# Kernel optimization log

Hardware: AMD Instinct MI355X
Metric: run time of the kernel (lower is better)

The kernel has to match this reference:

```python
import jax, jax.numpy as jnp
import numpy as np

DIM, NH, HD = 512, 16, 32   # dim, num_heads, head_dim = dim // num_heads
WH, WW = 8, 8               # window_size
SCALE = HD ** -0.5


def _rope2(t):
    """Axial 2D rotary embedding. t: (M, WH, WW, HD). First HD/2 dims rotate
    with the height position, last HD/2 with the width position."""
    d = HD // 2
    inv_freq = 1.0 / (10000.0 ** (jnp.arange(0, d, 2, dtype=jnp.float32) / d))  # (d/2,)

    def cos_sin(n):
        ang = jnp.arange(n, dtype=jnp.float32)[:, None] * inv_freq              # (n, d/2)
        return (jnp.concatenate([jnp.cos(ang)] * 2, -1),
                jnp.concatenate([jnp.sin(ang)] * 2, -1))                        # (n, d)

    def rot_half(u):
        u1, u2 = jnp.split(u, 2, axis=-1)
        return jnp.concatenate([-u2, u1], -1)

    cos_h, sin_h = cos_sin(WH)
    cos_w, sin_w = cos_sin(WW)
    th, tw = t[..., :d], t[..., d:]
    th = th * cos_h[:, None, :] + rot_half(th) * sin_h[:, None, :]
    tw = tw * cos_w[None, :, :] + rot_half(tw) * sin_w[None, :, :]
    return jnp.concatenate([th, tw], -1)


def setup_inputs() -> dict:
    key = jax.random.key(0)
    ks = jax.random.split(key, 8)
    s = 0.02
    return {
        "x": jax.random.normal(ks[0], (8, 64, 64, DIM), dtype=jnp.float32),
        "qkv_w": jax.random.normal(ks[1], (DIM, 3 * DIM), dtype=jnp.float32) * s,
        "qkv_b": jnp.zeros((3 * DIM,), dtype=jnp.float32),
        "kv_w": jax.random.normal(ks[2], (DIM, 2 * DIM), dtype=jnp.float32) * s,
        "kv_b": jnp.zeros((2 * DIM,), dtype=jnp.float32),
        "proj_w": jax.random.normal(ks[3], (DIM, DIM), dtype=jnp.float32) * s,
        "proj_b": jnp.zeros((DIM,), dtype=jnp.float32),
    }


def reference(x, qkv_w, qkv_b, kv_w, kv_b, proj_w, proj_b):
    B, H, W, C = x.shape
    # --- hydra linear-attention branch (computed in the torch module even when
    # use_attn=True, but its result is discarded on that path) ---
    hy_k, hy_v = jnp.split(x @ kv_w + kv_b, 2, axis=-1)
    hy_k = hy_k / jnp.linalg.norm(hy_k, axis=-1, keepdims=True)
    hy_kv = (hy_k * hy_v).reshape(B, -1, C).sum(axis=-2, keepdims=True)  # (B,1,C), unused (use_attn=True)

    # --- window partition: (B,H,W,C) -> (B*nW, N, C), N = WH*WW ---
    xw = (x.reshape(B, H // WH, WH, W // WW, WW, C)
           .transpose(0, 1, 3, 2, 4, 5)
           .reshape(-1, WH * WW, C))
    B_, N, _ = xw.shape

    qkv = (xw @ qkv_w + qkv_b).reshape(B_, N, 3, NH, HD).transpose(2, 0, 3, 1, 4)
    q, k, v = qkv[0], qkv[1], qkv[2]                 # each (B_, NH, N, HD)

    q = _rope2(q.reshape(-1, WH, WW, HD)).reshape(B_, NH, N, HD)
    k = _rope2(k.reshape(-1, WH, WW, HD)).reshape(B_, NH, N, HD)

    attn = jax.nn.softmax(jnp.einsum('bhnd,bhmd->bhnm', q * SCALE, k), axis=-1)
    out = jnp.einsum('bhnm,bhmd->bhnd', attn, v)     # (B_, NH, N, HD)
    out = out.transpose(0, 2, 1, 3).reshape(B_, N, C)

    # --- window reverse: (B*nW, N, C) -> (B, H*W, C) ---
    out = (out.reshape(B, H // WH, W // WW, WH, WW, C)
              .transpose(0, 1, 3, 2, 4, 5)
              .reshape(B, H * W, C))

    out = out @ proj_w + proj_b
    return out.reshape(B, H, W, C)
```

## Files before the change

### kernel.cpp

```cpp
#include <hip/hip_runtime.h>
#include <cstdint>
#include <cstddef>

typedef float v4f  __attribute__((ext_vector_type(4)));
typedef __bf16 v8bf __attribute__((ext_vector_type(8)));
typedef __bf16 v4bf __attribute__((ext_vector_type(4)));

#define M_TOT 32768
#define KDIM  512
#define NQKV  1536
#define NPROJ 512

__device__ __constant__ float c_invf[8] = {
  1.f, 0.31622776601683794f, 0.1f, 0.031622776601683794f,
  0.01f, 0.0031622776601683794f, 0.001f, 0.00031622776601683794f };

__device__ __forceinline__ void async_copy16(const void* g, void* l) {
  __builtin_amdgcn_global_load_lds((const __attribute__((address_space(1))) void*)g,
                                   (__attribute__((address_space(3))) void*)l, 16, 0, 0);
}

__global__ void cast_x_kernel(const float* __restrict__ in, __bf16* __restrict__ out, int n8) {
  for (int i = blockIdx.x * blockDim.x + threadIdx.x; i < n8; i += gridDim.x * blockDim.x) {
    const float4* p = (const float4*)in + (size_t)i * 2;
    float4 a = p[0], b = p[1];
    v8bf r = { (__bf16)a.x, (__bf16)a.y, (__bf16)a.z, (__bf16)a.w,
               (__bf16)b.x, (__bf16)b.y, (__bf16)b.z, (__bf16)b.w };
    *(v8bf*)(out + (size_t)i * 8) = r;
  }
}

__global__ __launch_bounds__(256) void transpose_cast_kernel(
    const float* __restrict__ w, __bf16* __restrict__ wt, int K, int N) {
  __shared__ __bf16 t[64 * 72];
  const int tid = threadIdx.x;
  const int n0 = blockIdx.x * 64, k0 = blockIdx.y * 64;
#pragma unroll
  for (int i = 0; i < 16; ++i) {
    int e = i * 256 + tid;
    int kk = e >> 6, nn = e & 63;
    t[nn * 72 + kk] = (__bf16)w[(size_t)(k0 + kk) * N + n0 + nn];
  }
  __syncthreads();
#pragma unroll
  for (int i = 0; i < 2; ++i) {
    int e = i * 256 + tid;
    int nn = e >> 3, kc = e & 7;
    *(v8bf*)&wt[(size_t)(n0 + nn) * K + k0 + kc * 8] = *(const v8bf*)&t[nn * 72 + kc * 8];
  }
}

#define REG_STRIDE 12288

__global__ __launch_bounds__(256, 3) void gemm_qkv_attn(
    const __bf16* __restrict__ A,
    const __bf16* __restrict__ Bt,
    const float* __restrict__ bias,
    __bf16* __restrict__ attn_out)
{
  __shared__ __align__(16) char smem[49152];
  __bf16* As = (__bf16*)smem;
  __bf16* Bs = (__bf16*)(smem + 16384);

  const int tid  = threadIdx.x;
  const int lane = tid & 63;
  const int wave = tid >> 6;
  const int lrow = lane & 15, quad = lane >> 4;
  const int hp   = blockIdx.y & 7;
  const int mt   = (blockIdx.y & ~7) | blockIdx.x;
  const int wl   = wave >> 1, hl = wave & 1;
  const int head = hp * 2 + hl;

  int mbase[2];
#pragma unroll
  for (int l = 0; l < 2; ++l) {
    int w  = mt * 2 + l;
    int b  = w >> 6, Wr = (w >> 3) & 7, Wc = w & 7;
    mbase[l] = b * 4096 + Wr * 512 + Wc * 8;
  }

  const __bf16* aptr[4]; __bf16* adst[4];
  const __bf16* bptr[6]; __bf16* bdst[6];
#pragma unroll
  for (int i = 0; i < 4; ++i) {
    int s = i * 256 + tid;
    int row = s >> 3, c = s & 7, qc = c ^ (row & 7);
    int tok = row & 63;
    int m = mbase[row >> 6] + ((tok >> 3) << 6) + (tok & 7);
    aptr[i] = A + (size_t)m * KDIM + qc * 8;
    adst[i] = &As[(i * 256 + (tid & ~63)) * 8];
  }
#pragma unroll
  for (int i = 0; i < 6; ++i) {
    int s = i * 256 + tid;
    int rl = s >> 3, c = s & 7, qc = c ^ (rl & 7);
    int sel = rl >> 6, rem = rl & 63;
    int grow = sel * 512 + (hp * 2 + (rem >> 5)) * 32 + (rem & 31);
    bptr[i] = Bt + (size_t)grow * KDIM + qc * 8;
    bdst[i] = &Bs[(i * 256 + (tid & ~63)) * 8];
  }

  v4f acc[4][6] = {};

  for (int k0 = 0; k0 < KDIM; k0 += 64) {
#pragma unroll
    for (int i = 0; i < 4; ++i) { async_copy16(aptr[i], adst[i]); aptr[i] += 64; }
#pragma unroll
    for (int i = 0; i < 6; ++i) { async_copy16(bptr[i], bdst[i]); bptr[i] += 64; }
    __syncthreads();
#pragma unroll
    for (int kb = 0; kb < 2; ++kb) {
      int sx = (((kb << 2) | quad) ^ (lrow & 7)) * 8;
      v8bf af[4], bfr[6];
#pragma unroll
      for (int mi = 0; mi < 4; ++mi)
        af[mi] = *(const v8bf*)&As[(wl * 64 + mi * 16 + lrow) * 64 + sx];
#pragma unroll
      for (int j = 0; j < 6; ++j)
        bfr[j] = *(const v8bf*)&Bs[((j >> 1) * 64 + hl * 32 + (j & 1) * 16 + lrow) * 64 + sx];
#pragma unroll
      for (int mi = 0; mi < 4; ++mi)
#pragma unroll
        for (int j = 0; j < 6; ++j)
          acc[mi][j] = __builtin_amdgcn_mfma_f32_16x16x32_bf16(af[mi], bfr[j], acc[mi][j], 0, 0, 0);
    }
    __syncthreads();
  }

  __bf16* reg = (__bf16*)(smem + wave * REG_STRIDE);
  __bf16* qL = reg;
  __bf16* kL = reg + 64 * 32;
  __bf16* vL = reg + 2 * 64 * 32;

  {
    const float invf = c_invf[lrow & 7];
    float cvh[4], svh[4], cvw[4], svw[4];
#pragma unroll
    for (int mi = 0; mi < 4; ++mi)
      __sincosf((float)(mi * 2 + (quad >> 1)) * invf, &svh[mi], &cvh[mi]);
#pragma unroll
    for (int r = 0; r < 4; ++r)
      __sincosf((float)((quad & 1) * 4 + r) * invf, &svw[r], &cvw[r]);

#pragma unroll
    for (int j = 0; j < 4; ++j) {
      int sel = j >> 1, nh = j & 1;
      int hd  = nh * 16 + lrow;
      int g   = nh * 2 + (lrow >> 3);
      float bv = bias[sel * 512 + head * 32 + hd];
      __bf16* dst = sel ? kL : qL;
#pragma unroll
      for (int mi = 0; mi < 4; ++mi) {
#pragma unroll
        for (int r = 0; r < 4; ++r) {
          int tok = mi * 16 + quad * 4 + r;
          float val = acc[mi][j][r] + bv;
          float partner = __shfl_xor(val, 8);
          float cv = nh ? cvw[r] : cvh[mi];
          float sv = nh ? svw[r] : svh[mi];
          float rh = (lrow & 8) ? partner : -partner;
          val = val * cv + rh * sv;
          if (sel == 0) val *= 0.17677669529663689f;
          dst[tok * 32 + ((g ^ quad) << 3) + (lrow & 7)] = (__bf16)val;
        }
      }
    }
  }
#pragma unroll
  for (int j = 4; j < 6; ++j) {
    int hd = (j - 4) * 16 + lrow;
    float bv = bias[1024 + head * 32 + hd];
#pragma unroll
    for (int mi = 0; mi < 4; ++mi) {
      v4bf pk;
#pragma unroll
      for (int r = 0; r < 4; ++r) pk[r] = (__bf16)(acc[mi][j][r] + bv);
      int gt = mi * 2 + (quad >> 1);
      *(v4bf*)&vL[hd * 64 + ((gt ^ (lrow & 7)) << 3) + (quad & 1) * 4] = pk;
    }
  }

  const int sq = (quad ^ (lrow >> 2)) << 3;
  v8bf qf[4], kf[4];
#pragma unroll
  for (int mi = 0; mi < 4; ++mi)
    qf[mi] = *(const v8bf*)&qL[(mi * 16 + lrow) * 32 + sq];
#pragma unroll
  for (int ni = 0; ni < 4; ++ni)
    kf[ni] = *(const v8bf*)&kL[(ni * 16 + lrow) * 32 + sq];

  v4f S[4][4] = {};
#pragma unroll
  for (int ni = 0; ni < 4; ++ni)
#pragma unroll
    for (int mi = 0; mi < 4; ++mi)
      S[ni][mi] = __builtin_amdgcn_mfma_f32_16x16x32_bf16(kf[ni], qf[mi], S[ni][mi], 0, 0, 0);

#pragma unroll
  for (int mi = 0; mi < 4; ++mi) {
    float mx = S[0][mi][0];
#pragma unroll
    for (int ni = 0; ni < 4; ++ni)
#pragma unroll
      for (int r = 0; r < 4; ++r) mx = fmaxf(mx, S[ni][mi][r]);
    mx = fmaxf(mx, __shfl_xor(mx, 16));
    mx = fmaxf(mx, __shfl_xor(mx, 32));
    float sum = 0.f;
#pragma unroll
    for (int ni = 0; ni < 4; ++ni)
#pragma unroll
      for (int r = 0; r < 4; ++r) {
        float e = __expf(S[ni][mi][r] - mx);
        S[ni][mi][r] = e; sum += e;
      }
    sum += __shfl_xor(sum, 16);
    sum += __shfl_xor(sum, 32);
    float inv = 1.f / sum;
#pragma unroll
    for (int ni = 0; ni < 4; ++ni)
#pragma unroll
      for (int r = 0; r < 4; ++r) S[ni][mi][r] *= inv;
  }

  __bf16* P = reg;
#pragma unroll
  for (int mi = 0; mi < 4; ++mi) {
    int q = mi * 16 + lrow;
#pragma unroll
    for (int ni = 0; ni < 4; ++ni) {
      v4bf pk;
#pragma unroll
      for (int r = 0; r < 4; ++r) pk[r] = (__bf16)S[ni][mi][r];
      int g = ni * 2 + (quad >> 1);
      *(v4bf*)&P[q * 64 + ((g ^ (lrow & 7)) << 3) + (quad & 1) * 4] = pk;
    }
  }

  v8bf pf[4][2], vf[2][2];
#pragma unroll
  for (int mi = 0; mi < 4; ++mi)
#pragma unroll
    for (int kc = 0; kc < 2; ++kc) {
      int row = mi * 16 + lrow;
      pf[mi][kc] = *(const v8bf*)&P[row * 64 + (((kc * 4 + quad) ^ (lrow & 7)) << 3)];
    }
#pragma unroll
  for (int kc = 0; kc < 2; ++kc)
#pragma unroll
    for (int nj = 0; nj < 2; ++nj) {
      int hd = nj * 16 + lrow;
      vf[kc][nj] = *(const v8bf*)&vL[hd * 64 + (((kc * 4 + quad) ^ (lrow & 7)) << 3)];
    }

  v4f o[2][4] = {};
#pragma unroll
  for (int nj = 0; nj < 2; ++nj)
#pragma unroll
    for (int mi = 0; mi < 4; ++mi)
#pragma unroll
      for (int kc = 0; kc < 2; ++kc)
        o[nj][mi] = __builtin_amdgcn_mfma_f32_16x16x32_bf16(vf[kc][nj], pf[mi][kc], o[nj][mi], 0, 0, 0);

  const int gwin = mt * 2 + wl;
#pragma unroll
  for (int mi = 0; mi < 4; ++mi) {
    size_t rowoff = ((size_t)gwin * 64 + mi * 16 + lrow) * 512 + head * 32 + quad * 4;
#pragma unroll
    for (int nj = 0; nj < 2; ++nj) {
      v4bf pk;
#pragma unroll
      for (int r = 0; r < 4; ++r) pk[r] = (__bf16)o[nj][mi][r];
      *(v4bf*)&attn_out[rowoff + nj * 16] = pk;
    }
  }
}

__global__ __launch_bounds__(256, 3) void gemm_proj(
    const __bf16* __restrict__ A,
    const __bf16* __restrict__ Bt,
    const float* __restrict__ bias,
    float* __restrict__ out)
{
  __shared__ __align__(16) char smem[32768];
  __bf16* As = (__bf16*)smem;
  __bf16* Bs = (__bf16*)(smem + 16384);
  const int tid  = threadIdx.x;
  const int lane = tid & 63;
  const int wave = tid >> 6;
  const int lrow = lane & 15, quad = lane >> 4;

  const int lin = blockIdx.x + blockIdx.y * 4;
  const int xcd = lin & 7, idx = lin >> 3;
  const int m0  = (xcd * 32 + (idx >> 2)) * 128;
  const int n0  = (idx & 3) * 128;

  const __bf16* aptr[4]; __bf16* adst[4];
  const __bf16* bptr[4]; __bf16* bdst[4];
#pragma unroll
  for (int i = 0; i < 4; ++i) {
    int s = i * 256 + tid;
    int row = s >> 3, c = s & 7, qc = c ^ (row & 7);
    aptr[i] = A + (size_t)(m0 + row) * KDIM + qc * 8;
    adst[i] = &As[(i * 256 + (tid & ~63)) * 8];
    bptr[i] = Bt + (size_t)(n0 + row) * KDIM + qc * 8;
    bdst[i] = &Bs[(i * 256 + (tid & ~63)) * 8];
  }

  v4f acc[8][2] = {};

  for (int k0 = 0; k0 < KDIM; k0 += 64) {
#pragma unroll
    for (int i = 0; i < 4; ++i) { async_copy16(aptr[i], adst[i]); aptr[i] += 64; }
#pragma unroll
    for (int i = 0; i < 4; ++i) { async_copy16(bptr[i], bdst[i]); bptr[i] += 64; }
    __syncthreads();
#pragma unroll
    for (int kb = 0; kb < 2; ++kb) {
      int sx = (((kb << 2) | quad) ^ (lrow & 7)) * 8;
      v8bf af[2], bfr[8];
#pragma unroll
      for (int mi = 0; mi < 2; ++mi)
        af[mi] = *(const v8bf*)&As[(wave * 32 + mi * 16 + lrow) * 64 + sx];
#pragma unroll
      for (int ni = 0; ni < 8; ++ni)
        bfr[ni] = *(const v8bf*)&Bs[(ni * 16 + lrow) * 64 + sx];
#pragma unroll
      for (int ni = 0; ni < 8; ++ni)
#pragma unroll
        for (int mi = 0; mi < 2; ++mi)
          acc[ni][mi] = __builtin_amdgcn_mfma_f32_16x16x32_bf16(bfr[ni], af[mi], acc[ni][mi], 0, 0, 0);
    }
    __syncthreads();
  }

  float4 bv[8];
#pragma unroll
  for (int ni = 0; ni < 8; ++ni)
    bv[ni] = *(const float4*)&bias[n0 + ni * 16 + quad * 4];

  const int mb = m0 + wave * 32;
#pragma unroll
  for (int mi = 0; mi < 2; ++mi) {
    int m    = mb + mi * 16 + lrow;
    int win  = m >> 6, tok = m & 63;
    int bb   = win >> 6;
    int hblk = (win >> 3) & 7, wblk = win & 7;
    int h    = hblk * 8 + (tok >> 3);
    int w    = wblk * 8 + (tok & 7);
    float* orow = &out[(((size_t)bb * 64 + h) * 64 + w) * 512 + n0 + quad * 4];
#pragma unroll
    for (int ni = 0; ni < 8; ++ni) {
      float4 v = { acc[ni][mi][0] + bv[ni].x, acc[ni][mi][1] + bv[ni].y,
                   acc[ni][mi][2] + bv[ni].z, acc[ni][mi][3] + bv[ni].w };
      *(float4*)&orow[ni * 16] = v;
    }
  }
}

extern "C" void kernel_launch(void* const* d_in, const int* in_sizes, int n_in,
                              void* d_out, int out_size, void* d_ws, size_t ws_size,
                              hipStream_t stream) {
  (void)in_sizes; (void)n_in; (void)out_size; (void)ws_size;
  const float* x      = (const float*)d_in[0];
  const float* qkv_w  = (const float*)d_in[1];
  const float* qkv_b  = (const float*)d_in[2];
  const float* proj_w = (const float*)d_in[5];
  const float* proj_b = (const float*)d_in[6];
  float* out = (float*)d_out;

  char* ws = (char*)d_ws;
  size_t off = 0;
  auto alloc = [&](size_t bytes) {
    char* p = ws + off;
    off += (bytes + 255) & ~(size_t)255;
    return (void*)p;
  };
  __bf16* xb       = (__bf16*)alloc((size_t)M_TOT * KDIM * 2);
  __bf16* qkv_wt   = (__bf16*)alloc((size_t)NQKV * KDIM * 2);
  __bf16* proj_wt  = (__bf16*)alloc((size_t)KDIM * KDIM * 2);
  __bf16* attn_out = (__bf16*)alloc((size_t)M_TOT * KDIM * 2);

  cast_x_kernel<<<dim3(2048), dim3(256), 0, stream>>>(
      x, xb, M_TOT * KDIM / 8);
  transpose_cast_kernel<<<dim3(NQKV / 64, KDIM / 64), dim3(256), 0, stream>>>(
      qkv_w, qkv_wt, KDIM, NQKV);
  transpose_cast_kernel<<<dim3(NPROJ / 64, KDIM / 64), dim3(256), 0, stream>>>(
      proj_w, proj_wt, KDIM, NPROJ);

  gemm_qkv_attn<<<dim3(8, 256), dim3(256), 0, stream>>>(
      xb, qkv_wt, qkv_b, attn_out);

  gemm_proj<<<dim3(4, 256), dim3(256), 0, stream>>>(
      attn_out, proj_wt, proj_b, out);
}
```

Before: 219.8 us.

## Double-buffer K-loop LDS tiles with prefetch in QKV-attn and proj GEMMs

Both GEMM kernels now run their K loop in 32-wide steps with two LDS buffers: the next step's tiles are issued with async global-to-LDS copies while the current tile is consumed, which removes one of the two barriers per iteration. Tiles use a packed two-rows-per-64-element layout with a new XOR swizzle, and the MFMA block is wrapped in s_setprio to favour the compute waves. gemm_proj's launch bounds rise to 4 blocks per CU, which tightens the register budget. Iterations double in count with less work each, and the new swizzle and indexing risk bank conflicts or mistakes.

```diff
diff --git a/kernel.cpp b/kernel.cpp
--- a/kernel.cpp
+++ b/kernel.cpp
@@ -59,8 +59,7 @@
     __bf16* __restrict__ attn_out)
 {
   __shared__ __align__(16) char smem[49152];
-  __bf16* As = (__bf16*)smem;
-  __bf16* Bs = (__bf16*)(smem + 16384);
+  __bf16* smemb = (__bf16*)smem;
 
   const int tid  = threadIdx.x;
   const int lane = tid & 63;
@@ -79,53 +78,70 @@
     mbase[l] = b * 4096 + Wr * 512 + Wc * 8;
   }
 
-  const __bf16* aptr[4]; __bf16* adst[4];
-  const __bf16* bptr[6]; __bf16* bdst[6];
-#pragma unroll
-  for (int i = 0; i < 4; ++i) {
-    int s = i * 256 + tid;
-    int row = s >> 3, c = s & 7, qc = c ^ (row & 7);
-    int tok = row & 63;
-    int m = mbase[row >> 6] + ((tok >> 3) << 6) + (tok & 7);
-    aptr[i] = A + (size_t)m * KDIM + qc * 8;
-    adst[i] = &As[(i * 256 + (tid & ~63)) * 8];
-  }
-#pragma unroll
-  for (int i = 0; i < 6; ++i) {
-    int s = i * 256 + tid;
-    int rl = s >> 3, c = s & 7, qc = c ^ (rl & 7);
-    int sel = rl >> 6, rem = rl & 63;
+  const __bf16* aptr[2]; int adst[2];
+  const __bf16* bptr[3]; int bdst[3];
+#pragma unroll
+  for (int i = 0; i < 2; ++i) {
+    int chunk = i * 256 + tid;
+    int row2 = chunk >> 3, slot = chunk & 7;
+    int g = slot ^ (row2 & 7);
+    int trow = row2 * 2 + (g >> 2), kgrp = g & 3;
+    int tok = trow & 63;
+    int m = mbase[trow >> 6] + ((tok >> 3) << 6) + (tok & 7);
+    aptr[i] = A + (size_t)m * KDIM + kgrp * 8;
+    adst[i] = (i * 256 + (tid & ~63)) * 8;
+  }
+#pragma unroll
+  for (int i = 0; i < 3; ++i) {
+    int chunk = i * 256 + tid;
+    int row2 = chunk >> 3, slot = chunk & 7;
+    int g = slot ^ (row2 & 7);
+    int trow = row2 * 2 + (g >> 2), kgrp = g & 3;
+    int sel = trow >> 6, rem = trow & 63;
     int grow = sel * 512 + (hp * 2 + (rem >> 5)) * 32 + (rem & 31);
-    bptr[i] = Bt + (size_t)grow * KDIM + qc * 8;
-    bdst[i] = &Bs[(i * 256 + (tid & ~63)) * 8];
-  }
+    bptr[i] = Bt + (size_t)grow * KDIM + kgrp * 8;
+    bdst[i] = 4096 + (i * 256 + (tid & ~63)) * 8;
+  }
+
+#pragma unroll
+  for (int i = 0; i < 2; ++i) async_copy16(aptr[i], smemb + adst[i]);
+#pragma unroll
+  for (int i = 0; i < 3; ++i) async_copy16(bptr[i], smemb + bdst[i]);
 
   v4f acc[4][6] = {};
-
-  for (int k0 = 0; k0 < KDIM; k0 += 64) {
-#pragma unroll
-    for (int i = 0; i < 4; ++i) { async_copy16(aptr[i], adst[i]); aptr[i] += 64; }
-#pragma unroll
-    for (int i = 0; i < 6; ++i) { async_copy16(bptr[i], bdst[i]); bptr[i] += 64; }
+  const int slot8 = ((((lrow & 1) << 2) | quad) ^ (lrow >> 1)) << 3;
+  const int arow2 = wl * 32 + (lrow >> 1);
+  const int brow2 = hl * 16 + (lrow >> 1);
+
+#pragma unroll
+  for (int t = 0; t < 16; ++t) {
     __syncthreads();
-#pragma unroll
-    for (int kb = 0; kb < 2; ++kb) {
-      int sx = (((kb << 2) | quad) ^ (lrow & 7)) * 8;
-      v8bf af[4], bfr[6];
-#pragma unroll
-      for (int mi = 0; mi < 4; ++mi)
-        af[mi] = *(const v8bf*)&As[(wl * 64 + mi * 16 + lrow) * 64 + sx];
+    if (t < 15) {
+      int nb  = ((t + 1) & 1) * 10240;
+      int kof = (t + 1) * 32;
+#pragma unroll
+      for (int i = 0; i < 2; ++i) async_copy16(aptr[i] + kof, smemb + nb + adst[i]);
+#pragma unroll
+      for (int i = 0; i < 3; ++i) async_copy16(bptr[i] + kof, smemb + nb + bdst[i]);
+    }
+    const __bf16* Ac = smemb + (t & 1) * 10240;
+    const __bf16* Bc = Ac + 4096;
+    v8bf af[4], bfr[6];
+#pragma unroll
+    for (int mi = 0; mi < 4; ++mi)
+      af[mi] = *(const v8bf*)&Ac[(arow2 + mi * 8) * 64 + slot8];
+#pragma unroll
+    for (int j = 0; j < 6; ++j)
+      bfr[j] = *(const v8bf*)&Bc[((j >> 1) * 32 + (j & 1) * 8 + brow2) * 64 + slot8];
+    __builtin_amdgcn_s_setprio(1);
+#pragma unroll
+    for (int mi = 0; mi < 4; ++mi)
 #pragma unroll
       for (int j = 0; j < 6; ++j)
-        bfr[j] = *(const v8bf*)&Bs[((j >> 1) * 64 + hl * 32 + (j & 1) * 16 + lrow) * 64 + sx];
-#pragma unroll
-      for (int mi = 0; mi < 4; ++mi)
-#pragma unroll
-        for (int j = 0; j < 6; ++j)
-          acc[mi][j] = __builtin_amdgcn_mfma_f32_16x16x32_bf16(af[mi], bfr[j], acc[mi][j], 0, 0, 0);
-    }
-    __syncthreads();
-  }
+        acc[mi][j] = __builtin_amdgcn_mfma_f32_16x16x32_bf16(af[mi], bfr[j], acc[mi][j], 0, 0, 0);
+    __builtin_amdgcn_s_setprio(0);
+  }
+  __syncthreads();
 
   __bf16* reg = (__bf16*)(smem + wave * REG_STRIDE);
   __bf16* qL = reg;
@@ -275,15 +291,14 @@
   }
 }
 
-__global__ __launch_bounds__(256, 3) void gemm_proj(
+__global__ __launch_bounds__(256, 4) void gemm_proj(
     const __bf16* __restrict__ A,
     const __bf16* __restrict__ Bt,
     const float* __restrict__ bias,
     float* __restrict__ out)
 {
   __shared__ __align__(16) char smem[32768];
-  __bf16* As = (__bf16*)smem;
-  __bf16* Bs = (__bf16*)(smem + 16384);
+  __bf16* smemb = (__bf16*)smem;
   const int tid  = threadIdx.x;
   const int lane = tid & 63;
   const int wave = tid >> 6;
@@ -294,43 +309,57 @@
   const int m0  = (xcd * 32 + (idx >> 2)) * 128;
   const int n0  = (idx & 3) * 128;
 
-  const __bf16* aptr[4]; __bf16* adst[4];
-  const __bf16* bptr[4]; __bf16* bdst[4];
-#pragma unroll
-  for (int i = 0; i < 4; ++i) {
-    int s = i * 256 + tid;
-    int row = s >> 3, c = s & 7, qc = c ^ (row & 7);
-    aptr[i] = A + (size_t)(m0 + row) * KDIM + qc * 8;
-    adst[i] = &As[(i * 256 + (tid & ~63)) * 8];
-    bptr[i] = Bt + (size_t)(n0 + row) * KDIM + qc * 8;
-    bdst[i] = &Bs[(i * 256 + (tid & ~63)) * 8];
+  const __bf16* aptr[2]; const __bf16* bptr[2]; int adst[2], bdst[2];
+#pragma unroll
+  for (int i = 0; i < 2; ++i) {
+    int chunk = i * 256 + tid;
+    int row2 = chunk >> 3, slot = chunk & 7;
+    int g = slot ^ (row2 & 7);
+    int trow = row2 * 2 + (g >> 2), kgrp = g & 3;
+    aptr[i] = A + (size_t)(m0 + trow) * KDIM + kgrp * 8;
+    bptr[i] = Bt + (size_t)(n0 + trow) * KDIM + kgrp * 8;
+    adst[i] = (i * 256 + (tid & ~63)) * 8;
+    bdst[i] = 4096 + adst[i];
+  }
+
+#pragma unroll
+  for (int i = 0; i < 2; ++i) {
+    async_copy16(aptr[i], smemb + adst[i]);
+    async_copy16(bptr[i], smemb + bdst[i]);
   }
 
   v4f acc[8][2] = {};
-
-  for (int k0 = 0; k0 < KDIM; k0 += 64) {
-#pragma unroll
-    for (int i = 0; i < 4; ++i) { async_copy16(aptr[i], adst[i]); aptr[i] += 64; }
-#pragma unroll
-    for (int i = 0; i < 4; ++i) { async_copy16(bptr[i], bdst[i]); bptr[i] += 64; }
+  const int slot8 = ((((lrow & 1) << 2) | quad) ^ (lrow >> 1)) << 3;
+  const int lr2 = lrow >> 1;
+
+#pragma unroll
+  for (int t = 0; t < 16; ++t) {
     __syncthreads();
-#pragma unroll
-    for (int kb = 0; kb < 2; ++kb) {
-      int sx = (((kb << 2) | quad) ^ (lrow & 7)) * 8;
-      v8bf af[2], bfr[8];
+    if (t < 15) {
+      int nb  = ((t + 1) & 1) * 8192;
+      int kof = (t + 1) * 32;
+#pragma unroll
+      for (int i = 0; i < 2; ++i) {
+        async_copy16(aptr[i] + kof, smemb + nb + adst[i]);
+        async_copy16(bptr[i] + kof, smemb + nb + bdst[i]);
+      }
+    }
+    const __bf16* Ac = smemb + (t & 1) * 8192;
+    const __bf16* Bc = Ac + 4096;
+    v8bf af[2], bfr[8];
+#pragma unroll
+    for (int mi = 0; mi < 2; ++mi)
+      af[mi] = *(const v8bf*)&Ac[(wave * 16 + mi * 8 + lr2) * 64 + slot8];
+#pragma unroll
+    for (int ni = 0; ni < 8; ++ni)
+      bfr[ni] = *(const v8bf*)&Bc[(ni * 8 + lr2) * 64 + slot8];
+    __builtin_amdgcn_s_setprio(1);
+#pragma unroll
+    for (int ni = 0; ni < 8; ++ni)
 #pragma unroll
       for (int mi = 0; mi < 2; ++mi)
-        af[mi] = *(const v8bf*)&As[(wave * 32 + mi * 16 + lrow) * 64 + sx];
-#pragma unroll
-      for (int ni = 0; ni < 8; ++ni)
-        bfr[ni] = *(const v8bf*)&Bs[(ni * 16 + lrow) * 64 + sx];
-#pragma unroll
-      for (int ni = 0; ni < 8; ++ni)
-#pragma unroll
-        for (int mi = 0; mi < 2; ++mi)
-          acc[ni][mi] = __builtin_amdgcn_mfma_f32_16x16x32_bf16(bfr[ni], af[mi], acc[ni][mi], 0, 0, 0);
-    }
-    __syncthreads();
+        acc[ni][mi] = __builtin_amdgcn_mfma_f32_16x16x32_bf16(bfr[ni], af[mi], acc[ni][mi], 0, 0, 0);
+    __builtin_amdgcn_s_setprio(0);
   }
 
   float4 bv[8];
```

Measured after the change: 223.3 us. Within noise of the previous version (+1.6%).

## Fuse x fp32-to-bf16 cast into QKV GEMM and double-buffer proj GEMM

Applied to the files above, without the earlier changes.

Removes the separate cast kernel and the bf16 copy of x. The QKV+attention kernel now loads fp32 x directly, converts it in registers and writes it to LDS. This saves a full write and read pass over the activation, but the A-tile loads become synchronous register loads rather than async LDS copies. Separately, the projection GEMM is restructured to use a double-buffered 32-wide K tile with prefetch, a new swizzle, MFMA priority hints and launch bounds raised to 4 blocks per unit.

```diff
diff --git a/kernel.cpp b/kernel.cpp
--- a/kernel.cpp
+++ b/kernel.cpp
@@ -18,16 +18,6 @@
 __device__ __forceinline__ void async_copy16(const void* g, void* l) {
   __builtin_amdgcn_global_load_lds((const __attribute__((address_space(1))) void*)g,
                                    (__attribute__((address_space(3))) void*)l, 16, 0, 0);
-}
-
-__global__ void cast_x_kernel(const float* __restrict__ in, __bf16* __restrict__ out, int n8) {
-  for (int i = blockIdx.x * blockDim.x + threadIdx.x; i < n8; i += gridDim.x * blockDim.x) {
-    const float4* p = (const float4*)in + (size_t)i * 2;
-    float4 a = p[0], b = p[1];
-    v8bf r = { (__bf16)a.x, (__bf16)a.y, (__bf16)a.z, (__bf16)a.w,
-               (__bf16)b.x, (__bf16)b.y, (__bf16)b.z, (__bf16)b.w };
-    *(v8bf*)(out + (size_t)i * 8) = r;
-  }
 }
 
 __global__ __launch_bounds__(256) void transpose_cast_kernel(
@@ -53,7 +43,7 @@
 #define REG_STRIDE 12288
 
 __global__ __launch_bounds__(256, 3) void gemm_qkv_attn(
-    const __bf16* __restrict__ A,
+    const float* __restrict__ X,
     const __bf16* __restrict__ Bt,
     const float* __restrict__ bias,
     __bf16* __restrict__ attn_out)
@@ -79,7 +69,7 @@
     mbase[l] = b * 4096 + Wr * 512 + Wc * 8;
   }
 
-  const __bf16* aptr[4]; __bf16* adst[4];
+  const float4* aptrf[4]; int aoff[4];
   const __bf16* bptr[6]; __bf16* bdst[6];
 #pragma unroll
   for (int i = 0; i < 4; ++i) {
@@ -87,8 +77,8 @@
     int row = s >> 3, c = s & 7, qc = c ^ (row & 7);
     int tok = row & 63;
     int m = mbase[row >> 6] + ((tok >> 3) << 6) + (tok & 7);
-    aptr[i] = A + (size_t)m * KDIM + qc * 8;
-    adst[i] = &As[(i * 256 + (tid & ~63)) * 8];
+    aptrf[i] = (const float4*)(X + (size_t)m * KDIM) + qc * 2;
+    aoff[i]  = (i * 256 + tid) * 8;
   }
 #pragma unroll
   for (int i = 0; i < 6; ++i) {
@@ -103,10 +93,17 @@
   v4f acc[4][6] = {};
 
   for (int k0 = 0; k0 < KDIM; k0 += 64) {
-#pragma unroll
-    for (int i = 0; i < 4; ++i) { async_copy16(aptr[i], adst[i]); aptr[i] += 64; }
+    float4 av0[4], av1[4];
+#pragma unroll
+    for (int i = 0; i < 4; ++i) { av0[i] = aptrf[i][0]; av1[i] = aptrf[i][1]; aptrf[i] += 16; }
 #pragma unroll
     for (int i = 0; i < 6; ++i) { async_copy16(bptr[i], bdst[i]); bptr[i] += 64; }
+#pragma unroll
+    for (int i = 0; i < 4; ++i) {
+      v8bf r = { (__bf16)av0[i].x, (__bf16)av0[i].y, (__bf16)av0[i].z, (__bf16)av0[i].w,
+                 (__bf16)av1[i].x, (__bf16)av1[i].y, (__bf16)av1[i].z, (__bf16)av1[i].w };
+      *(v8bf*)&As[aoff[i]] = r;
+    }
     __syncthreads();
 #pragma unroll
     for (int kb = 0; kb < 2; ++kb) {
@@ -275,15 +272,14 @@
   }
 }
 
-__global__ __launch_bounds__(256, 3) void gemm_proj(
+__global__ __launch_bounds__(256, 4) void gemm_proj(
     const __bf16* __restrict__ A,
     const __bf16* __restrict__ Bt,
     const float* __restrict__ bias,
     float* __restrict__ out)
 {
   __shared__ __align__(16) char smem[32768];
-  __bf16* As = (__bf16*)smem;
-  __bf16* Bs = (__bf16*)(smem + 16384);
+  __bf16* smemb = (__bf16*)smem;
   const int tid  = threadIdx.x;
   const int lane = tid & 63;
   const int wave = tid >> 6;
@@ -294,43 +290,57 @@
   const int m0  = (xcd * 32 + (idx >> 2)) * 128;
   const int n0  = (idx & 3) * 128;
 
-  const __bf16* aptr[4]; __bf16* adst[4];
-  const __bf16* bptr[4]; __bf16* bdst[4];
-#pragma unroll
-  for (int i = 0; i < 4; ++i) {
-    int s = i * 256 + tid;
-    int row = s >> 3, c = s & 7, qc = c ^ (row & 7);
-    aptr[i] = A + (size_t)(m0 + row) * KDIM + qc * 8;
-    adst[i] = &As[(i * 256 + (tid & ~63)) * 8];
-    bptr[i] = Bt + (size_t)(n0 + row) * KDIM + qc * 8;
-    bdst[i] = &Bs[(i * 256 + (tid & ~63)) * 8];
+  const __bf16* aptr[2]; const __bf16* bptr[2]; int adst[2], bdst[2];
+#pragma unroll
+  for (int i = 0; i < 2; ++i) {
+    int chunk = i * 256 + tid;
+    int row2 = chunk >> 3, slot = chunk & 7;
+    int g = slot ^ (row2 & 7);
+    int trow = row2 * 2 + (g >> 2), kgrp = g & 3;
+    aptr[i] = A + (size_t)(m0 + trow) * KDIM + kgrp * 8;
+    bptr[i] = Bt + (size_t)(n0 + trow) * KDIM + kgrp * 8;
+    adst[i] = (i * 256 + (tid & ~63)) * 8;
+    bdst[i] = 4096 + adst[i];
+  }
+
+#pragma unroll
+  for (int i = 0; i < 2; ++i) {
+    async_copy16(aptr[i], smemb + adst[i]);
+    async_copy16(bptr[i], smemb + bdst[i]);
   }
 
   v4f acc[8][2] = {};
-
-  for (int k0 = 0; k0 < KDIM; k0 += 64) {
-#pragma unroll
-    for (int i = 0; i < 4; ++i) { async_copy16(aptr[i], adst[i]); aptr[i] += 64; }
-#pragma unroll
-    for (int i = 0; i < 4; ++i) { async_copy16(bptr[i], bdst[i]); bptr[i] += 64; }
+  const int slot8 = ((((lrow & 1) << 2) | quad) ^ (lrow >> 1)) << 3;
+  const int lr2 = lrow >> 1;
+
+#pragma unroll
+  for (int t = 0; t < 16; ++t) {
     __syncthreads();
-#pragma unroll
-    for (int kb = 0; kb < 2; ++kb) {
-      int sx = (((kb << 2) | quad) ^ (lrow & 7)) * 8;
-      v8bf af[2], bfr[8];
+    if (t < 15) {
+      int nb  = ((t + 1) & 1) * 8192;
+      int kof = (t + 1) * 32;
+#pragma unroll
+      for (int i = 0; i < 2; ++i) {
+        async_copy16(aptr[i] + kof, smemb + nb + adst[i]);
+        async_copy16(bptr[i] + kof, smemb + nb + bdst[i]);
+      }
+    }
+    const __bf16* Ac = smemb + (t & 1) * 8192;
+    const __bf16* Bc = Ac + 4096;
+    v8bf af[2], bfr[8];
+#pragma unroll
+    for (int mi = 0; mi < 2; ++mi)
+      af[mi] = *(const v8bf*)&Ac[(wave * 16 + mi * 8 + lr2) * 64 + slot8];
+#pragma unroll
+    for (int ni = 0; ni < 8; ++ni)
+      bfr[ni] = *(const v8bf*)&Bc[(ni * 8 + lr2) * 64 + slot8];
+    __builtin_amdgcn_s_setprio(1);
+#pragma unroll
+    for (int ni = 0; ni < 8; ++ni)
 #pragma unroll
       for (int mi = 0; mi < 2; ++mi)
-        af[mi] = *(const v8bf*)&As[(wave * 32 + mi * 16 + lrow) * 64 + sx];
-#pragma unroll
-      for (int ni = 0; ni < 8; ++ni)
-        bfr[ni] = *(const v8bf*)&Bs[(ni * 16 + lrow) * 64 + sx];
-#pragma unroll
-      for (int ni = 0; ni < 8; ++ni)
-#pragma unroll
-        for (int mi = 0; mi < 2; ++mi)
-          acc[ni][mi] = __builtin_amdgcn_mfma_f32_16x16x32_bf16(bfr[ni], af[mi], acc[ni][mi], 0, 0, 0);
-    }
-    __syncthreads();
+        acc[ni][mi] = __builtin_amdgcn_mfma_f32_16x16x32_bf16(bfr[ni], af[mi], acc[ni][mi], 0, 0, 0);
+    __builtin_amdgcn_s_setprio(0);
   }
 
   float4 bv[8];
@@ -375,20 +385,17 @@
     off += (bytes + 255) & ~(size_t)255;
     return (void*)p;
   };
-  __bf16* xb       = (__bf16*)alloc((size_t)M_TOT * KDIM * 2);
   __bf16* qkv_wt   = (__bf16*)alloc((size_t)NQKV * KDIM * 2);
   __bf16* proj_wt  = (__bf16*)alloc((size_t)KDIM * KDIM * 2);
   __bf16* attn_out = (__bf16*)alloc((size_t)M_TOT * KDIM * 2);
 
-  cast_x_kernel<<<dim3(2048), dim3(256), 0, stream>>>(
-      x, xb, M_TOT * KDIM / 8);
   transpose_cast_kernel<<<dim3(NQKV / 64, KDIM / 64), dim3(256), 0, stream>>>(
       qkv_w, qkv_wt, KDIM, NQKV);
   transpose_cast_kernel<<<dim3(NPROJ / 64, KDIM / 64), dim3(256), 0, stream>>>(
       proj_w, proj_wt, KDIM, NPROJ);
 
   gemm_qkv_attn<<<dim3(8, 256), dim3(256), 0, stream>>>(
-      xb, qkv_wt, qkv_b, attn_out);
+      x, qkv_wt, qkv_b, attn_out);
 
   gemm_proj<<<dim3(4, 256), dim3(256), 0, stream>>>(
       attn_out, proj_wt, proj_b, out);
```

Result: no change. 223.5 us (+1.7%).
